# Optimization experiments

Hardware: AMD Instinct MI355X
Metric: run time of the kernel (lower is better)

The kernel has to match this reference:

```python
import jax, jax.numpy as jnp
import numpy as np

B, S, E, H = 4, 2048, 1024, 16
D = E // H  # head dim = 64


def setup_inputs() -> dict:
    key = jax.random.key(0)
    ks = jax.random.split(key, 9)
    sc = 1.0 / np.sqrt(E)
    x = jax.random.normal(ks[0], (B, S, E), dtype=jnp.float32)
    # causal mask: 1 = keep, 0 = masked -> -inf (matches masked_fill(mask==0, -inf))
    mask = jnp.broadcast_to(jnp.tril(jnp.ones((S, S), dtype=jnp.int32)), (B, S, S))
    return {
        "x": x,
        "mask": mask,
        "wq": jax.random.normal(ks[1], (E, E), dtype=jnp.float32) * sc,
        "bq": jax.random.normal(ks[2], (E,), dtype=jnp.float32) * sc,
        "wk": jax.random.normal(ks[3], (E, E), dtype=jnp.float32) * sc,
        "bk": jax.random.normal(ks[4], (E,), dtype=jnp.float32) * sc,
        "wv": jax.random.normal(ks[5], (E, E), dtype=jnp.float32) * sc,
        "bv": jax.random.normal(ks[6], (E,), dtype=jnp.float32) * sc,
        "wo": jax.random.normal(ks[7], (E, E), dtype=jnp.float32) * sc,
        "bo": jax.random.normal(ks[8], (E,), dtype=jnp.float32) * sc,
    }


def reference(x, mask, wq, bq, wk, bk, wv, bv, wo, bo):
    # nn.Linear: y = x @ W^T + b
    def proj(w, b):
        y = jnp.einsum('bse,fe->bsf', x, w) + b
        return y.reshape(B, S, H, D).transpose(0, 2, 1, 3)  # [B,H,S,D]

    q = proj(wq, bq)
    k = proj(wk, bk)
    v = proj(wv, bv)
    denom = jnp.asarray(np.sqrt(D), dtype=x.dtype)
    score = jnp.einsum('bhqd,bhkd->bhqk', q, k) / denom  # [B,H,S,S]
    score = jnp.where(mask[:, None, :, :] == 0, jnp.asarray(-jnp.inf, score.dtype), score)
    attn = jax.nn.softmax(score, axis=-1)
    out = jnp.einsum('bhqk,bhkd->bhqd', attn, v)  # [B,H,S,D]
    out = out.transpose(0, 2, 1, 3).reshape(B, S, E)
    return jnp.einsum('bse,fe->bsf', out, wo) + bo
```

## Files before the change

kernel.cpp:

```cpp
#include <hip/hip_runtime.h>
#include <cstdint>
#include <cstddef>

typedef unsigned short u16;
typedef __bf16 bf16;
typedef bf16 bf16x8 __attribute__((ext_vector_type(8)));
typedef bf16 bf16x4 __attribute__((ext_vector_type(4)));
typedef float f32x4 __attribute__((ext_vector_type(4)));
typedef u16 u16x8 __attribute__((ext_vector_type(8)));
typedef u16 u16x4 __attribute__((ext_vector_type(4)));

#define ASYNC16(g, l) __builtin_amdgcn_global_load_lds( \
    (const __attribute__((address_space(1))) void*)(g), \
    (__attribute__((address_space(3))) void*)(l), 16, 0, 0)

__device__ __forceinline__ u16 f2bf(float f) {
  bf16 h = (bf16)f;
  return __builtin_bit_cast(u16, h);
}

__device__ __forceinline__ u16x4 pk4(float a, float b, float c, float d) {
  bf16x4 v = { (bf16)a, (bf16)b, (bf16)c, (bf16)d };
  return __builtin_bit_cast(u16x4, v);
}

__device__ __forceinline__ void store_out(u16* p, float v) { *p = f2bf(v); }
__device__ __forceinline__ void store_out(float* p, float v) { *p = v; }

__device__ __forceinline__ f32x4 mfma16(bf16x8 a, bf16x8 b, f32x4 c) {
  return __builtin_amdgcn_mfma_f32_16x16x32_bf16(a, b, c, 0, 0, 0);
}

__global__ void prep(const float* __restrict__ x,  const float* __restrict__ wq,
                     const float* __restrict__ wk, const float* __restrict__ wv,
                     const float* __restrict__ wo, const float* __restrict__ bq,
                     const float* __restrict__ bk,
                     u16* __restrict__ xb, u16* __restrict__ wqkb,
                     u16* __restrict__ wvb, u16* __restrict__ wob,
                     float* __restrict__ bqk, float scl)
{
  const int bid = blockIdx.x, tid = threadIdx.x;
  if (bid < 8192) {
    int i = bid * 256 + tid;
    float4 v = ((const float4*)x)[i];
    ((u16x4*)xb)[i] = pk4(v.x, v.y, v.z, v.w);
  } else if (bid < 12288) {
    int wsel = (bid - 8192) >> 10;
    int i = ((bid - 8192) & 1023) * 256 + tid;
    const float* src = wsel == 0 ? wq : wsel == 1 ? wk : wsel == 2 ? wv : wo;
    u16* dst = wsel == 0 ? wqkb : wsel == 1 ? wqkb + 1048576 : wsel == 2 ? wvb : wob;
    float s = wsel == 0 ? scl : 1.0f;
    float4 v = ((const float4*)src)[i];
    ((u16x4*)dst)[i] = pk4(v.x * s, v.y * s, v.z * s, v.w * s);
  } else {
    for (int i = tid; i < 1024; i += 256) {
      bqk[i] = bq[i] * scl;
      bqk[1024 + i] = bk[i];
    }
  }
}

template <typename OutT>
__device__ __forceinline__ void gemm_core(
    u16* As, u16* Bs,
    const u16* __restrict__ A, const u16* __restrict__ Bm,
    const float* __restrict__ bias_col, const float* __restrict__ bias_row,
    OutT* __restrict__ C, int M, int N, int K, int bm, int bn)
{
  const int tid = threadIdx.x;
  const int w = tid >> 6, lane = tid & 63;
  const int q = lane >> 4, l15 = lane & 15;
  const int wr = w >> 1, wc = w & 1;

  const u16* gA = A + (size_t)(bm * 128 + w * 32 + (lane >> 2)) * K + (lane & 3) * 8;
  const u16* gB = Bm + (size_t)(bn * 128 + w * 32 + (lane >> 2)) * K + (lane & 3) * 8;
  u16* lA = As + w * 32 * 32;
  u16* lB = Bs + w * 32 * 32;

  f32x4 acc[4][4] = {};

  for (int k0 = 0; k0 < K; k0 += 32) {
    ASYNC16(gA + k0,          lA);
    ASYNC16(gA + k0 + 16 * K, lA + 16 * 32);
    ASYNC16(gB + k0,          lB);
    ASYNC16(gB + k0 + 16 * K, lB + 16 * 32);
    __syncthreads();
    bf16x8 af[4], bfr[4];
#pragma unroll
    for (int mt = 0; mt < 4; mt++)
      af[mt] = *(const bf16x8*)(As + (wr * 64 + mt * 16 + l15) * 32 + q * 8);
#pragma unroll
    for (int nt = 0; nt < 4; nt++)
      bfr[nt] = *(const bf16x8*)(Bs + (wc * 64 + nt * 16 + l15) * 32 + q * 8);
#pragma unroll
    for (int mt = 0; mt < 4; mt++)
#pragma unroll
      for (int nt = 0; nt < 4; nt++)
        acc[mt][nt] = mfma16(af[mt], bfr[nt], acc[mt][nt]);
    __syncthreads();
  }

#pragma unroll
  for (int nt = 0; nt < 4; nt++) {
    int c = bn * 128 + wc * 64 + nt * 16 + l15;
    float bc = bias_col ? bias_col[c] : 0.f;
#pragma unroll
    for (int mt = 0; mt < 4; mt++) {
      int r0 = bm * 128 + wr * 64 + mt * 16 + q * 4;
      f32x4 v = acc[mt][nt];
#pragma unroll
      for (int ri = 0; ri < 4; ri++) {
        float bv = bc + (bias_row ? bias_row[r0 + ri] : 0.f);
        store_out(&C[(size_t)(r0 + ri) * N + c], v[ri] + bv);
      }
    }
  }
}

template <typename OutT>
__global__ __launch_bounds__(256, 2) void gemm_bt(
    const u16* __restrict__ A, const u16* __restrict__ Bm,
    const float* __restrict__ bias_col, const float* __restrict__ bias_row,
    OutT* __restrict__ C, int M, int N, int K)
{
  __shared__ u16 As[128 * 32];
  __shared__ u16 Bs[128 * 32];
  gemm_core<OutT>(As, Bs, A, Bm, bias_col, bias_row, C, M, N, K,
                  blockIdx.x, blockIdx.y);
}

__global__ __launch_bounds__(256, 2) void gemm_qkv(
    const u16* __restrict__ xb, const u16* __restrict__ wqkb,
    const u16* __restrict__ wvb, const float* __restrict__ bqk,
    const float* __restrict__ bv, u16* __restrict__ qk, u16* __restrict__ vt)
{
  __shared__ u16 As[128 * 32];
  __shared__ u16 Bs[128 * 32];
  const int id = blockIdx.x;
  if (id < 1024)
    gemm_core<u16>(As, Bs, xb, wqkb, bqk, nullptr, qk, 8192, 2048, 1024,
                   id & 63, id >> 6);
  else {
    const int j = id - 1024;
    gemm_core<u16>(As, Bs, wvb, xb, nullptr, bv, vt, 1024, 8192, 1024,
                   j & 7, j >> 3);
  }
}

__global__ __launch_bounds__(512, 2) void fattn(
    const u16* __restrict__ QK, const u16* __restrict__ VT, u16* __restrict__ ctx)
{
  __shared__ u16 Kt[128 * 64];
  __shared__ u16 Vt[64 * 128];
  __shared__ u16 Pt[8 * 32 * 64];

  const int tid = threadIdx.x;
  const int w = tid >> 6, lane = tid & 63;
  const int quad = lane >> 4, l15 = lane & 15;
  const int bx = blockIdx.x, h = blockIdx.y, b = blockIdx.z;
  const int P8[8] = {7, 0, 6, 1, 5, 2, 4, 3};
  const int tq = (b & 2) ? 7 - P8[bx] : P8[bx];
  const int qbase = tq * 256 + w * 32;

  const int kr = tid >> 3, kc = (tid & 7) ^ (kr & 7);
  const int vr = tid >> 4, vc = (tid & 15) ^ (vr & 15);

  const u16* QKb = QK + (size_t)b * 2048 * 2048;
  const u16* Kg = QKb + 1024 + h * 64 + kc * 8;
  const u16* Vg = VT + (size_t)(h * 64) * 8192 + b * 2048 + vc * 8;

  u16* Pw = Pt + w * 2048;

  bf16x8 ones;
#pragma unroll
  for (int j = 0; j < 8; j++) ones[j] = (bf16)1.0f;

  bf16x8 qf[2][2];
#pragma unroll
  for (int mt = 0; mt < 2; mt++)
#pragma unroll
    for (int ks = 0; ks < 2; ks++)
      qf[mt][ks] = *(const bf16x8*)(QKb + (size_t)(qbase + mt * 16 + l15) * 2048 +
                                    h * 64 + ks * 32 + quad * 8);

  f32x4 oacc[4][2] = {};
  f32x4 lacc[2] = {};

  const int tmax = 2 * tq + 1;
  for (int t = 0; t <= tmax; t++) {
    __syncthreads();
#pragma unroll
    for (int s = 0; s < 2; s++) {
      ASYNC16(Kg + (size_t)(t * 128 + s * 64 + kr) * 2048, Kt + (s * 512 + w * 64) * 8);
      ASYNC16(Vg + (size_t)(s * 32 + vr) * 8192 + t * 128,  Vt + (s * 512 + w * 64) * 8);
    }
    __syncthreads();

    f32x4 st[2][8] = {};
#pragma unroll
    for (int ks = 0; ks < 2; ks++) {
      bf16x8 kf[8];
#pragma unroll
      for (int nt = 0; nt < 8; nt++) {
        int row = nt * 16 + l15;
        kf[nt] = *(const bf16x8*)(Kt + (row * 8 + ((ks * 4 + quad) ^ (row & 7))) * 8);
      }
#pragma unroll
      for (int nt = 0; nt < 8; nt++) {
        st[0][nt] = mfma16(kf[nt], qf[0][ks], st[0][nt]);
        st[1][nt] = mfma16(kf[nt], qf[1][ks], st[1][nt]);
      }
    }

    if (t >= 2 * tq) {
#pragma unroll
      for (int mt = 0; mt < 2; mt++) {
        const int qg = qbase + mt * 16 + l15;
#pragma unroll
        for (int nt = 0; nt < 8; nt++)
#pragma unroll
          for (int r = 0; r < 4; r++)
            if (t * 128 + nt * 16 + quad * 4 + r > qg) st[mt][nt][r] = -3e38f;
      }
    }
#pragma unroll
    for (int mt = 0; mt < 2; mt++)
#pragma unroll
      for (int nt = 0; nt < 8; nt++)
#pragma unroll
        for (int r = 0; r < 4; r++)
          st[mt][nt][r] = exp2f(st[mt][nt][r]);

#pragma unroll
    for (int hf = 0; hf < 2; hf++) {
#pragma unroll
      for (int mt = 0; mt < 2; mt++) {
        const int row = mt * 16 + l15;
#pragma unroll
        for (int n2 = 0; n2 < 4; n2++) {
          int nt = hf * 4 + n2;
          u16x4 pk = pk4(st[mt][nt][0], st[mt][nt][1], st[mt][nt][2], st[mt][nt][3]);
          int c = n2 * 2 + (quad >> 1);
          *(u16x4*)(Pw + (row << 6) + ((c ^ (row & 7)) << 3) + ((quad & 1) << 2)) = pk;
        }
      }
#pragma unroll
      for (int ks = 0; ks < 2; ks++) {
        const int c = ks * 4 + quad;
        bf16x8 pf0 = *(const bf16x8*)(Pw + (l15 << 6) + ((c ^ (l15 & 7)) << 3));
        bf16x8 pf1 = *(const bf16x8*)(Pw + ((16 + l15) << 6) + ((c ^ (l15 & 7)) << 3));
        lacc[0] = mfma16(ones, pf0, lacc[0]);
        lacc[1] = mfma16(ones, pf1, lacc[1]);
#pragma unroll
        for (int dt = 0; dt < 4; dt++) {
          int row = dt * 16 + l15;
          bf16x8 vf = *(const bf16x8*)(Vt + (row * 16 + ((hf * 8 + ks * 4 + quad) ^ (row & 15))) * 8);
          oacc[dt][0] = mfma16(vf, pf0, oacc[dt][0]);
          oacc[dt][1] = mfma16(vf, pf1, oacc[dt][1]);
        }
      }
    }
  }

#pragma unroll
  for (int mt = 0; mt < 2; mt++) {
    float rl = 1.0f / lacc[mt][0];
    size_t row = (size_t)b * 2048 + qbase + mt * 16 + l15;
#pragma unroll
    for (int dt = 0; dt < 4; dt++) {
      u16x4 o = pk4(oacc[dt][mt][0] * rl, oacc[dt][mt][1] * rl,
                    oacc[dt][mt][2] * rl, oacc[dt][mt][3] * rl);
      *(u16x4*)(ctx + row * 1024 + h * 64 + dt * 16 + quad * 4) = o;
    }
  }
}

extern "C" void kernel_launch(void* const* d_in, const int* in_sizes, int n_in,
                              void* d_out, int out_size, void* d_ws, size_t ws_size,
                              hipStream_t stream)
{
  const float* x  = (const float*)d_in[0];
  const float* wq = (const float*)d_in[2];
  const float* bq = (const float*)d_in[3];
  const float* wk = (const float*)d_in[4];
  const float* bk = (const float*)d_in[5];
  const float* wv = (const float*)d_in[6];
  const float* bv = (const float*)d_in[7];
  const float* wo = (const float*)d_in[8];
  const float* bo = (const float*)d_in[9];

  const float SCL = 0.125f * 1.44269504088896f;

  char* ws = (char*)d_ws;
  u16*   xb   = (u16*)(ws);
  u16*   ctx  = (u16*)(ws);
  u16*   wqkb = (u16*)(ws + 16777216);
  u16*   wvb  = (u16*)(ws + 20971520);
  u16*   wob  = (u16*)(ws + 23068672);
  float* bqk  = (float*)(ws + 25165824);
  u16*   qk   = (u16*)(ws + 25174016);
  u16*   vt   = (u16*)(ws + 58728448);
  float* out  = (float*)d_out;

  prep<<<12289, 256, 0, stream>>>(x, wq, wk, wv, wo, bq, bk,
                                  xb, wqkb, wvb, wob, bqk, SCL);

  gemm_qkv<<<1536, 256, 0, stream>>>(xb, wqkb, wvb, bqk, bv, qk, vt);
  fattn<<<dim3(8, 16, 4), 512, 0, stream>>>(qk, vt, ctx);
  gemm_bt<float><<<dim3(64, 8), 256, 0, stream>>>(ctx, wob, bo, nullptr, out, 8192, 1024, 1024);
}
```

Baseline: 320.5 us.

## Replace 128x128 GEMMs with pipelined 256x256 tile, 8-wave, double-buffered LDS GEMM

Rewrites the projection GEMM core as a 256x256 tile computed by 8 waves. It uses a BK=64 K-step with double-buffered, XOR-swizzled LDS, async global-to-LDS loads interleaved with MFMA quarter-phases, explicit vmcnt waits and raised wave priority during MFMA bursts. The goal is more data reuse per load, fewer LDS bank conflicts and load latency hidden behind compute, which the old single-buffer 128x128 loop with two barriers per 32-wide K-step did not provide. The cost is 128KB of LDS per block and far fewer blocks (384 and 128), which risks poor CU occupancy and tail effects, especially for the output projection.

```diff
diff --git a/kernel.cpp b/kernel.cpp
--- a/kernel.cpp
+++ b/kernel.cpp
@@ -13,6 +13,10 @@
 #define ASYNC16(g, l) __builtin_amdgcn_global_load_lds( \
     (const __attribute__((address_space(1))) void*)(g), \
     (__attribute__((address_space(3))) void*)(l), 16, 0, 0)
+
+#define FENCE asm volatile("" ::: "memory")
+#define BARRIER do { FENCE; __builtin_amdgcn_s_barrier(); FENCE; } while (0)
+#define WAITVM(n) asm volatile("s_waitcnt vmcnt(" #n ")" ::: "memory")
 
 __device__ __forceinline__ u16 f2bf(float f) {
   bf16 h = (bf16)f;
@@ -61,90 +65,183 @@
 }
 
 template <typename OutT>
-__device__ __forceinline__ void gemm_core(
-    u16* As, u16* Bs,
+__device__ __forceinline__ void gemm256(
+    u16* sA, u16* sB,
     const u16* __restrict__ A, const u16* __restrict__ Bm,
     const float* __restrict__ bias_col, const float* __restrict__ bias_row,
     OutT* __restrict__ C, int M, int N, int K, int bm, int bn)
 {
   const int tid = threadIdx.x;
   const int w = tid >> 6, lane = tid & 63;
-  const int q = lane >> 4, l15 = lane & 15;
-  const int wr = w >> 1, wc = w & 1;
-
-  const u16* gA = A + (size_t)(bm * 128 + w * 32 + (lane >> 2)) * K + (lane & 3) * 8;
-  const u16* gB = Bm + (size_t)(bn * 128 + w * 32 + (lane >> 2)) * K + (lane & 3) * 8;
-  u16* lA = As + w * 32 * 32;
-  u16* lB = Bs + w * 32 * 32;
-
-  f32x4 acc[4][4] = {};
-
-  for (int k0 = 0; k0 < K; k0 += 32) {
-    ASYNC16(gA + k0,          lA);
-    ASYNC16(gA + k0 + 16 * K, lA + 16 * 32);
-    ASYNC16(gB + k0,          lB);
-    ASYNC16(gB + k0 + 16 * K, lB + 16 * 32);
-    __syncthreads();
-    bf16x8 af[4], bfr[4];
-#pragma unroll
-    for (int mt = 0; mt < 4; mt++)
-      af[mt] = *(const bf16x8*)(As + (wr * 64 + mt * 16 + l15) * 32 + q * 8);
-#pragma unroll
-    for (int nt = 0; nt < 4; nt++)
-      bfr[nt] = *(const bf16x8*)(Bs + (wc * 64 + nt * 16 + l15) * 32 + q * 8);
-#pragma unroll
-    for (int mt = 0; mt < 4; mt++)
-#pragma unroll
-      for (int nt = 0; nt < 4; nt++)
-        acc[mt][nt] = mfma16(af[mt], bfr[nt], acc[mt][nt]);
-    __syncthreads();
+  const int quad = lane >> 4, l15 = lane & 15;
+  const int wr = w >> 2, wc = w & 3;
+
+  const int srow = tid >> 3;
+  const int sslot = (tid & 7) ^ (srow & 7);
+  const u16* gA = A + (size_t)(bm * 256 + srow) * K + sslot * 8;
+  const u16* gB = Bm + (size_t)(bn * 256 + srow) * K + sslot * 8;
+  u16* dA = sA + tid * 8;
+  u16* dB = sB + tid * 8;
+  const size_t rK64 = (size_t)64 * K, rK128 = (size_t)128 * K;
+
+  auto stageA = [&](int c, int h, int kt) {
+    const u16* s = gA + h * rK128 + kt * 64;
+    u16* d = dA + c * 16384 + h * 8192;
+    ASYNC16(s, d);
+    ASYNC16(s + rK64, d + 4096);
+  };
+  auto stageB = [&](int c, int h, int kt) {
+    const u16* s = gB + h * rK128 + kt * 64;
+    u16* d = dB + c * 16384 + h * 8192;
+    ASYNC16(s, d);
+    ASYNC16(s + rK64, d + 4096);
+  };
+
+  f32x4 acc[8][4] = {};
+  bf16x8 af[4][2];
+  bf16x8 bf0[2][2];
+  bf16x8 bf1[2][2];
+
+  const int aRow = (wr * 128 + l15) * 64;
+  const int bRow = (wc * 64 + l15) * 64;
+  const int sw0 = (quad ^ (l15 & 7)) * 8;
+
+#define LDA8(SRC, MH) do { \
+    _Pragma("unroll") \
+    for (int i = 0; i < 4; i++) { \
+      af[i][0] = *(const bf16x8*)((SRC) + aRow + ((MH)*4 + i) * 1024 + sw0); \
+      af[i][1] = *(const bf16x8*)((SRC) + aRow + ((MH)*4 + i) * 1024 + (sw0 ^ 32)); \
+    } } while (0)
+
+#define LDB4(DST, SRC, NH) do { \
+    _Pragma("unroll") \
+    for (int j = 0; j < 2; j++) { \
+      DST[j][0] = *(const bf16x8*)((SRC) + bRow + ((NH)*2 + j) * 1024 + sw0); \
+      DST[j][1] = *(const bf16x8*)((SRC) + bRow + ((NH)*2 + j) * 1024 + (sw0 ^ 32)); \
+    } } while (0)
+
+#define MMQ(MH, NH, BF) do { \
+    __builtin_amdgcn_s_setprio(1); \
+    _Pragma("unroll") \
+    for (int i = 0; i < 4; i++) { \
+      acc[(MH)*4+i][(NH)*2+0] = mfma16(af[i][0], BF[0][0], acc[(MH)*4+i][(NH)*2+0]); \
+      acc[(MH)*4+i][(NH)*2+0] = mfma16(af[i][1], BF[0][1], acc[(MH)*4+i][(NH)*2+0]); \
+      acc[(MH)*4+i][(NH)*2+1] = mfma16(af[i][0], BF[1][0], acc[(MH)*4+i][(NH)*2+1]); \
+      acc[(MH)*4+i][(NH)*2+1] = mfma16(af[i][1], BF[1][1], acc[(MH)*4+i][(NH)*2+1]); \
+    } \
+    __builtin_amdgcn_s_setprio(0); \
+  } while (0)
+
+  const int NT = K >> 6, NI = NT >> 1;
+
+  stageB(0, 0, 0); stageB(0, 1, 0);
+  stageA(0, 0, 0); stageA(0, 1, 0);
+  stageB(1, 0, 1); stageB(1, 1, 1);
+  WAITVM(4);
+  BARRIER;
+
+  u16* sA0 = sA;         u16* sA1 = sA + 16384;
+  u16* sB0 = sB;         u16* sB1 = sB + 16384;
+
+  for (int t = 0; t < NI; ++t) {
+    const int k1 = 2 * t + 1, kn = 2 * t + 2, kn1 = 2 * t + 3;
+    const bool more = (t + 1 < NI);
+
+    LDA8(sA0, 0); LDB4(bf0, sB0, 0);
+    stageA(1, 0, k1);
+    BARRIER;
+    MMQ(0, 0, bf0);
+    BARRIER;
+
+    LDB4(bf1, sB0, 1);
+    stageA(1, 1, k1);
+    BARRIER;
+    MMQ(0, 1, bf1);
+    BARRIER;
+
+    LDA8(sA0, 1);
+    if (more) stageB(0, 0, kn);
+    BARRIER;
+    MMQ(1, 1, bf1);
+    BARRIER;
+
+    if (more) { stageB(0, 1, kn); WAITVM(4); }
+    else      { WAITVM(0); }
+    BARRIER;
+    MMQ(1, 0, bf0);
+    BARRIER;
+
+    LDA8(sA1, 0); LDB4(bf0, sB1, 0);
+    if (more) stageA(0, 0, kn);
+    BARRIER;
+    MMQ(0, 0, bf0);
+    BARRIER;
+
+    LDB4(bf1, sB1, 1);
+    if (more) stageA(0, 1, kn);
+    BARRIER;
+    MMQ(0, 1, bf1);
+    BARRIER;
+
+    LDA8(sA1, 1);
+    if (more) stageB(1, 0, kn1);
+    BARRIER;
+    MMQ(1, 1, bf1);
+    BARRIER;
+
+    if (more) { stageB(1, 1, kn1); WAITVM(4); }
+    BARRIER;
+    MMQ(1, 0, bf0);
+    BARRIER;
   }
 
 #pragma unroll
   for (int nt = 0; nt < 4; nt++) {
-    int c = bn * 128 + wc * 64 + nt * 16 + l15;
-    float bc = bias_col ? bias_col[c] : 0.f;
-#pragma unroll
-    for (int mt = 0; mt < 4; mt++) {
-      int r0 = bm * 128 + wr * 64 + mt * 16 + q * 4;
+    const int cc = bn * 256 + wc * 64 + nt * 16 + l15;
+    const float bc = bias_col ? bias_col[cc] : 0.f;
+#pragma unroll
+    for (int mt = 0; mt < 8; mt++) {
+      const int r0 = bm * 256 + wr * 128 + mt * 16 + quad * 4;
       f32x4 v = acc[mt][nt];
 #pragma unroll
       for (int ri = 0; ri < 4; ri++) {
-        float bv = bc + (bias_row ? bias_row[r0 + ri] : 0.f);
-        store_out(&C[(size_t)(r0 + ri) * N + c], v[ri] + bv);
-      }
-    }
-  }
-}
-
-template <typename OutT>
-__global__ __launch_bounds__(256, 2) void gemm_bt(
-    const u16* __restrict__ A, const u16* __restrict__ Bm,
-    const float* __restrict__ bias_col, const float* __restrict__ bias_row,
-    OutT* __restrict__ C, int M, int N, int K)
-{
-  __shared__ u16 As[128 * 32];
-  __shared__ u16 Bs[128 * 32];
-  gemm_core<OutT>(As, Bs, A, Bm, bias_col, bias_row, C, M, N, K,
-                  blockIdx.x, blockIdx.y);
-}
-
-__global__ __launch_bounds__(256, 2) void gemm_qkv(
+        const float bb = bc + (bias_row ? bias_row[r0 + ri] : 0.f);
+        store_out(&C[(size_t)(r0 + ri) * N + cc], v[ri] + bb);
+      }
+    }
+  }
+#undef LDA8
+#undef LDB4
+#undef MMQ
+}
+
+__global__ __launch_bounds__(512, 2) void gemm_qkv(
     const u16* __restrict__ xb, const u16* __restrict__ wqkb,
     const u16* __restrict__ wvb, const float* __restrict__ bqk,
     const float* __restrict__ bv, u16* __restrict__ qk, u16* __restrict__ vt)
 {
-  __shared__ u16 As[128 * 32];
-  __shared__ u16 Bs[128 * 32];
+  __shared__ __align__(16) u16 sA[2 * 16384];
+  __shared__ __align__(16) u16 sB[2 * 16384];
   const int id = blockIdx.x;
-  if (id < 1024)
-    gemm_core<u16>(As, Bs, xb, wqkb, bqk, nullptr, qk, 8192, 2048, 1024,
-                   id & 63, id >> 6);
-  else {
-    const int j = id - 1024;
-    gemm_core<u16>(As, Bs, wvb, xb, nullptr, bv, vt, 1024, 8192, 1024,
-                   j & 7, j >> 3);
-  }
+  if (id < 256) {
+    gemm256<u16>(sA, sB, xb, wqkb, bqk, nullptr, qk, 8192, 2048, 1024,
+                 id >> 3, id & 7);
+  } else {
+    const int j = id - 256, s = j >> 3;
+    gemm256<u16>(sA, sB, wvb, xb, nullptr, bv, vt, 1024, 8192, 1024,
+                 s & 3, (j & 7) * 4 + (s >> 2));
+  }
+}
+
+__global__ __launch_bounds__(512, 2) void gemm_out(
+    const u16* __restrict__ ctx, const u16* __restrict__ wob,
+    const float* __restrict__ bo, float* __restrict__ out)
+{
+  __shared__ __align__(16) u16 sA[2 * 16384];
+  __shared__ __align__(16) u16 sB[2 * 16384];
+  const int id = blockIdx.x, s = id >> 3;
+  gemm256<float>(sA, sB, ctx, wob, bo, nullptr, out, 8192, 1024, 1024,
+                 (id & 7) * 4 + (s >> 2), s & 3);
 }
 
 __global__ __launch_bounds__(512, 2) void fattn(
@@ -305,7 +402,7 @@
   prep<<<12289, 256, 0, stream>>>(x, wq, wk, wv, wo, bq, bk,
                                   xb, wqkb, wvb, wob, bqk, SCL);
 
-  gemm_qkv<<<1536, 256, 0, stream>>>(xb, wqkb, wvb, bqk, bv, qk, vt);
+  gemm_qkv<<<384, 512, 0, stream>>>(xb, wqkb, wvb, bqk, bv, qk, vt);
   fattn<<<dim3(8, 16, 4), 512, 0, stream>>>(qk, vt, ctx);
-  gemm_bt<float><<<dim3(64, 8), 256, 0, stream>>>(ctx, wob, bo, nullptr, out, 8192, 1024, 1024);
-}
+  gemm_out<<<128, 512, 0, stream>>>(ctx, wob, bo, out);
+}
```

New measurement: 326.9 us. +2.0%, slower.
